# Kernel optimization log

Hardware: AMD Instinct MI355X
Metric: run time of the kernel (lower is better)

Reference implementation:

```python
import jax, jax.numpy as jnp
import numpy as np

HID = 2048
HEADS = 16
HD = HID // HEADS  # 128
EPS = 1e-6


def setup_inputs() -> dict:
    key = jax.random.key(0)
    ks = jax.random.split(key, 9)
    s = 1.0 / np.sqrt(HID)
    return {
        "hidden_states": jax.random.normal(ks[0], (4, 4096, HID), jnp.float32),
        "q_w": jax.random.normal(ks[1], (HID, HID), jnp.float32) * s,
        "q_b": jnp.zeros((HID,), jnp.float32),
        "k_w": jax.random.normal(ks[2], (HID, HID), jnp.float32) * s,
        "k_b": jnp.zeros((HID,), jnp.float32),
        "v_w": jax.random.normal(ks[3], (HID, HID), jnp.float32) * s,
        "v_b": jnp.zeros((HID,), jnp.float32),
        "o_w": jax.random.normal(ks[4], (HID, HID), jnp.float32) * s,
        "o_b": jnp.zeros((HID,), jnp.float32),
    }


def _heads(x, b, s):
    # [B,S,HID] -> [B,H,S,Dh]
    return x.reshape(b, s, HEADS, HD).transpose(0, 2, 1, 3)


def reference(hidden_states, q_w, q_b, k_w, k_b, v_w, v_b, o_w, o_b):
    b, s, _ = hidden_states.shape
    # torch Linear: y = x @ W.T + b
    q = _heads(hidden_states @ q_w.T + q_b, b, s)
    k = _heads(hidden_states @ k_w.T + k_b, b, s)
    v = _heads(hidden_states @ v_w.T + v_b, b, s)
    # kernel feature map: elu(x) + 1
    qp = jax.nn.elu(q) + 1.0
    kp = jax.nn.elu(k) + 1.0
    # KV outer-product reduction over sequence: [B,H,Dh,Dh]
    kv = jnp.einsum('bhsd,bhse->bhde', kp, v)
    # normalizer z = q' @ sum_s k'  -> [B,H,S,1]
    z = jnp.einsum('bhsd,bhd->bhs', qp, kp.sum(axis=2))[..., None]
    attn = jnp.einsum('bhsd,bhde->bhse', qp, kv) / (z + EPS)
    out = attn.transpose(0, 2, 1, 3).reshape(b, s, HID)
    return out @ o_w.T + o_b
```

## Files before the change

### kernel.cpp

```cpp
#include <hip/hip_runtime.h>
#include <hip/hip_bf16.h>

#define HIDC 2048
#define NHEADS 16
#define HDIM 128
#define NB 4
#define NS 4096
#define NROWS (NB*NS)
#define QSTR 6144
#define EPSV 1e-6f

typedef __attribute__((ext_vector_type(8))) short s16x8;
typedef __attribute__((ext_vector_type(4))) float f32x4;
typedef __attribute__((ext_vector_type(8))) unsigned short u16x8;

static __device__ __forceinline__ unsigned short f2b(float f) {
  unsigned int u = __float_as_uint(f);
  u += 0x7fffu + ((u >> 16) & 1u);
  return (unsigned short)(u >> 16);
}
static __device__ __forceinline__ float b2f(unsigned short h) {
  return __uint_as_float(((unsigned int)h) << 16);
}

static __device__ __forceinline__ void gload_lds16(const unsigned short* g, unsigned short* l) {
  __builtin_amdgcn_global_load_lds(
      (const __attribute__((address_space(1))) void*)g,
      (__attribute__((address_space(3))) void*)l, 16, 0, 0);
}

__global__ __launch_bounds__(256) void convert_all(
    const float* __restrict__ hs, const float* __restrict__ qw,
    const float* __restrict__ kw, const float* __restrict__ vw,
    const float* __restrict__ ow,
    unsigned short* __restrict__ hsb, unsigned short* __restrict__ qwb,
    unsigned short* __restrict__ kwb, unsigned short* __restrict__ vwb,
    unsigned short* __restrict__ owb)
{
  int bid = blockIdx.x;
  const float* src; unsigned short* dst; size_t base;
  if (bid < 16384) { src = hs; dst = hsb; base = (size_t)bid << 11; }
  else {
    int t = bid - 16384; int wsel = t >> 11; int wb = t & 2047;
    src = wsel == 0 ? qw : wsel == 1 ? kw : wsel == 2 ? vw : ow;
    dst = wsel == 0 ? qwb : wsel == 1 ? kwb : wsel == 2 ? vwb : owb;
    base = (size_t)wb << 11;
  }
  size_t i = base + ((size_t)threadIdx.x << 3);
  float4 a = *(const float4*)(src + i);
  float4 b = *(const float4*)(src + i + 4);
  u16x8 o;
  o[0] = f2b(a.x); o[1] = f2b(a.y); o[2] = f2b(a.z); o[3] = f2b(a.w);
  o[4] = f2b(b.x); o[5] = f2b(b.y); o[6] = f2b(b.z); o[7] = f2b(b.w);
  *(u16x8*)(dst + i) = o;
}

template<int QKV, int OUT_BF16>
__global__ __launch_bounds__(512, 2) void gemm256(
    const unsigned short* __restrict__ A,
    const unsigned short* __restrict__ B0,
    const unsigned short* __restrict__ B1,
    const unsigned short* __restrict__ B2,
    const float* __restrict__ bias0,
    const float* __restrict__ bias1,
    const float* __restrict__ bias2,
    void* __restrict__ Cp,
    int ntile, int astr, int ostr)
{
  __shared__ unsigned short lds[65536];
  const int tid = threadIdx.x;
  const int lane = tid & 63, wid = tid >> 6;
  const int wr = wid >> 2, wc = wid & 3;
  const int l15 = lane & 15, l4 = lane >> 4;

  const int cpx = (int)gridDim.x >> 3;
  const int bidx = (int)blockIdx.x;
  const int wg = (bidx & 7) * cpx + (bidx >> 3);
  const int csz = ntile << 2;
  const int chunk = wg / csz;
  const int t = wg % csz;
  const int bm = ((chunk << 2) + (t & 3)) << 8;
  const int bn = (t >> 2) << 8;

  const unsigned short* Bp = B0;
  const float* bias = bias0;
  bool act = false;
  int bnw = bn;
  if (QKV) {
    int seg = bn >> 11;
    Bp = seg == 0 ? B0 : (seg == 1 ? B1 : B2);
    bias = seg == 0 ? bias0 : (seg == 1 ? bias1 : bias2);
    act = seg < 2;
    bnw = bn & 2047;
  }

  const int c0 = wid << 1;
  const int srow = lane >> 2;
  const int scol = (((lane & 3) ^ ((srow >> 1) & 3)) << 3);
  const unsigned short* Asrc0 = A + (size_t)(bm + (c0 << 4) + srow) * astr + scol;
  const unsigned short* Asrc1 = Asrc0 + (size_t)16 * astr;
  const unsigned short* Bsrc0 = Bp + (size_t)(bnw + (c0 << 4) + srow) * HIDC + scol;
  const unsigned short* Bsrc1 = Bsrc0 + (size_t)16 * HIDC;
  const int adst = c0 << 9;

  const int xa = ((l4 ^ ((l15 >> 1) & 3)) << 3);
  const int abase = ((wr << 7) + l15) * 32 + xa;
  const int bbase = 8192 + ((wc << 6) + l15) * 32 + xa;

  f32x4 acc[8][4] = {};
  s16x8 af[2][8];
  s16x8 bfr[4];

#define STAGE_A(s_) { const int sl_ = ((s_) & 3) << 14; const int kt_ = (s_) << 5; \
    gload_lds16(Asrc0 + kt_, &lds[sl_ + adst]); \
    gload_lds16(Asrc1 + kt_, &lds[sl_ + adst + 512]); }
#define STAGE_B(s_) { const int sl_ = ((s_) & 3) << 14; const int kt_ = (s_) << 5; \
    gload_lds16(Bsrc0 + kt_, &lds[sl_ + 8192 + adst]); \
    gload_lds16(Bsrc1 + kt_, &lds[sl_ + 8192 + adst + 512]); }

#define MM8(nf_, P_) { \
    acc[0][nf_] = __builtin_amdgcn_mfma_f32_16x16x32_bf16(af[P_][0], bfr[nf_], acc[0][nf_], 0, 0, 0); \
    acc[1][nf_] = __builtin_amdgcn_mfma_f32_16x16x32_bf16(af[P_][1], bfr[nf_], acc[1][nf_], 0, 0, 0); \
    acc[2][nf_] = __builtin_amdgcn_mfma_f32_16x16x32_bf16(af[P_][2], bfr[nf_], acc[2][nf_], 0, 0, 0); \
    acc[3][nf_] = __builtin_amdgcn_mfma_f32_16x16x32_bf16(af[P_][3], bfr[nf_], acc[3][nf_], 0, 0, 0); \
    acc[4][nf_] = __builtin_amdgcn_mfma_f32_16x16x32_bf16(af[P_][4], bfr[nf_], acc[4][nf_], 0, 0, 0); \
    acc[5][nf_] = __builtin_amdgcn_mfma_f32_16x16x32_bf16(af[P_][5], bfr[nf_], acc[5][nf_], 0, 0, 0); \
    acc[6][nf_] = __builtin_amdgcn_mfma_f32_16x16x32_bf16(af[P_][6], bfr[nf_], acc[6][nf_], 0, 0, 0); \
    acc[7][nf_] = __builtin_amdgcn_mfma_f32_16x16x32_bf16(af[P_][7], bfr[nf_], acc[7][nf_], 0, 0, 0); }

#define DO_STEP(s_, P_, GATE, DO_A, DO_STG) { \
    const int sl = ((s_) & 3) << 14; \
    if ((GATE) == 4)      { asm volatile("s_waitcnt vmcnt(4)" ::: "memory"); } \
    else if ((GATE) == 0) { asm volatile("s_waitcnt vmcnt(0)" ::: "memory"); } \
    __builtin_amdgcn_s_barrier(); \
    bfr[0] = *(const s16x8*)&lds[sl + bbase]; \
    bfr[1] = *(const s16x8*)&lds[sl + bbase + 512]; \
    bfr[2] = *(const s16x8*)&lds[sl + bbase + 1024]; \
    bfr[3] = *(const s16x8*)&lds[sl + bbase + 1536]; \
    if (DO_A) { \
      const int sln = (((s_) + 1) & 3) << 14; \
      af[1-(P_)][0] = *(const s16x8*)&lds[sln + abase]; \
      af[1-(P_)][1] = *(const s16x8*)&lds[sln + abase + 512]; \
      af[1-(P_)][2] = *(const s16x8*)&lds[sln + abase + 1024]; \
      af[1-(P_)][3] = *(const s16x8*)&lds[sln + abase + 1536]; \
      af[1-(P_)][4] = *(const s16x8*)&lds[sln + abase + 2048]; \
      af[1-(P_)][5] = *(const s16x8*)&lds[sln + abase + 2560]; \
      af[1-(P_)][6] = *(const s16x8*)&lds[sln + abase + 3072]; \
      af[1-(P_)][7] = *(const s16x8*)&lds[sln + abase + 3584]; \
    } \
    if (DO_STG) { STAGE_A((s_) + 3); STAGE_B((s_) + 3); } \
    __builtin_amdgcn_sched_barrier(0); \
    __builtin_amdgcn_s_setprio(1); \
    MM8(0, P_) MM8(1, P_) MM8(2, P_) MM8(3, P_) \
    __builtin_amdgcn_s_setprio(0); \
  }

  STAGE_A(0); STAGE_B(0);
  STAGE_A(1); STAGE_B(1);
  STAGE_A(2); STAGE_B(2);
  asm volatile("s_waitcnt vmcnt(8)" ::: "memory");
  __builtin_amdgcn_s_barrier();
  af[0][0] = *(const s16x8*)&lds[abase];
  af[0][1] = *(const s16x8*)&lds[abase + 512];
  af[0][2] = *(const s16x8*)&lds[abase + 1024];
  af[0][3] = *(const s16x8*)&lds[abase + 1536];
  af[0][4] = *(const s16x8*)&lds[abase + 2048];
  af[0][5] = *(const s16x8*)&lds[abase + 2560];
  af[0][6] = *(const s16x8*)&lds[abase + 3072];
  af[0][7] = *(const s16x8*)&lds[abase + 3584];

  for (int s = 0; s < 60; s += 2) {
    DO_STEP(s,     0, 4, 1, 1)
    DO_STEP(s + 1, 1, 4, 1, 1)
  }
  DO_STEP(60, 0, 4, 1, 1)
  DO_STEP(61, 1, 4, 1, 0)
  DO_STEP(62, 0, 0, 1, 0)
  DO_STEP(63, 1, -1, 0, 0)

#undef DO_STEP
#undef MM8
#undef STAGE_A
#undef STAGE_B

  #pragma unroll
  for (int nf = 0; nf < 4; ++nf) {
    const int colw = (wc << 6) + (nf << 4) + l15;
    const float bv = bias[bnw + colw];
    #pragma unroll
    for (int mf = 0; mf < 8; ++mf) {
      #pragma unroll
      for (int r = 0; r < 4; ++r) {
        const int row = bm + (wr << 7) + (mf << 4) + (l4 << 2) + r;
        float v = acc[mf][nf][r] + bv;
        if (QKV) { if (act) v = (v > 0.f) ? (v + 1.f) : __expf(v); }
        const size_t off = (size_t)row * ostr + bn + colw;
        if (OUT_BF16) ((unsigned short*)Cp)[off] = f2b(v);
        else          ((float*)Cp)[off] = v;
      }
    }
  }
}

__global__ __launch_bounds__(256) void kv_partial(
    const unsigned short* __restrict__ kp, const unsigned short* __restrict__ vv,
    float* __restrict__ kvp, float* __restrict__ ksp)
{
  const int bh = blockIdx.x >> 4;
  const int chunk = blockIdx.x & 15;
  const int b = bh >> 4, h = bh & 15;
  const int tid = threadIdx.x;
  const int td = tid >> 4, te = tid & 15;

  __shared__ float kpl[32][128];
  __shared__ float vl[32][132];

  float acc[8][8] = {};
  float ks[8] = {};

  const size_t rowbase = (size_t)b * NS * QSTR + (size_t)h * HDIM;
  const int s0 = chunk * 256;

  for (int st = 0; st < 256; st += 32) {
    __syncthreads();
    #pragma unroll
    for (int i = 0; i < 2; ++i) {
      int idx = tid + (i << 8);
      int row = idx >> 4, q = idx & 15;
      size_t g = rowbase + (size_t)(s0 + st + row) * QSTR + (q << 3);
      u16x8 k8 = *(const u16x8*)(kp + g);
      u16x8 v8 = *(const u16x8*)(vv + g);
      float tk[8], tv[8];
      #pragma unroll
      for (int j = 0; j < 8; ++j) { tk[j] = b2f(k8[j]); tv[j] = b2f(v8[j]); }
      *(float4*)&kpl[row][(q << 3)]     = make_float4(tk[0], tk[1], tk[2], tk[3]);
      *(float4*)&kpl[row][(q << 3) + 4] = make_float4(tk[4], tk[5], tk[6], tk[7]);
      *(float4*)&vl[row][(q << 3)]      = make_float4(tv[0], tv[1], tv[2], tv[3]);
      *(float4*)&vl[row][(q << 3) + 4]  = make_float4(tv[4], tv[5], tv[6], tv[7]);
    }
    __syncthreads();
    #pragma unroll 4
    for (int s = 0; s < 32; ++s) {
      float kd[8], ve[8];
      *(float4*)&kd[0] = *(const float4*)&kpl[s][td << 3];
      *(float4*)&kd[4] = *(const float4*)&kpl[s][(td << 3) + 4];
      *(float4*)&ve[0] = *(const float4*)&vl[s][te << 3];
      *(float4*)&ve[4] = *(const float4*)&vl[s][(te << 3) + 4];
      if (te == 0) {
        #pragma unroll
        for (int i = 0; i < 8; ++i) ks[i] += kd[i];
      }
      #pragma unroll
      for (int i = 0; i < 8; ++i)
        #pragma unroll
        for (int j = 0; j < 8; ++j)
          acc[i][j] += kd[i] * ve[j];
    }
  }

  float* outp = kvp + ((size_t)(chunk * 64 + bh) << 14);
  #pragma unroll
  for (int j = 0; j < 8; ++j) {
    int e = (te << 3) + j;
    float r0[8];
    #pragma unroll
    for (int i = 0; i < 8; ++i) r0[i] = acc[i][j];
    *(float4*)&outp[(size_t)e * HDIM + (td << 3)]     = *(float4*)&r0[0];
    *(float4*)&outp[(size_t)e * HDIM + (td << 3) + 4] = *(float4*)&r0[4];
  }
  if (te == 0) {
    float* kso = ksp + ((size_t)(chunk * 64 + bh) << 7) + (td << 3);
    #pragma unroll
    for (int i = 0; i < 8; ++i) kso[i] = ks[i];
  }
}

__global__ __launch_bounds__(256) void kv_reduce(
    const float* __restrict__ kvp, float* __restrict__ kvT)
{
  int i = blockIdx.x * 256 + threadIdx.x;
  float s = 0.f;
  #pragma unroll
  for (int c = 0; c < 16; ++c) s += kvp[(size_t)c * (64 * 16384) + i];
  kvT[i] = s;
}

__global__ __launch_bounds__(256) void attn_ker(
    const unsigned short* __restrict__ qp, const float* __restrict__ kvT,
    const float* __restrict__ ksp, unsigned short* __restrict__ attn)
{
  const int bh = blockIdx.x >> 5, stile = blockIdx.x & 31;
  const int b = bh >> 4, h = bh & 15;
  const int tid = threadIdx.x;
  const int lane = tid & 63, w = tid >> 6;
  const int l15 = lane & 15, l4 = lane >> 4;

  __shared__ unsigned short Qs[128][136];
  __shared__ unsigned short Ks[128][136];
  __shared__ float ksl[128];
  __shared__ float zs[128];

  const size_t qbase = ((size_t)b * NS + (size_t)stile * 128) * QSTR + (size_t)h * HDIM;

  #pragma unroll
  for (int i = 0; i < 8; ++i) {
    int idx = tid + (i << 8);
    int row = idx >> 4, q = idx & 15;
    u16x8 v8 = *(const u16x8*)(qp + qbase + (size_t)row * QSTR + (q << 3));
    *(u16x8*)&Qs[row][q << 3] = v8;
  }
  const float* kvb = kvT + ((size_t)bh << 14);
  #pragma unroll
  for (int i = 0; i < 16; ++i) {
    int idx = tid + (i << 8);
    int row = idx >> 5, q = idx & 31;
    float4 v4 = *(const float4*)(kvb + (size_t)row * HDIM + (q << 2));
    ushort4 w4; w4.x = f2b(v4.x); w4.y = f2b(v4.y); w4.z = f2b(v4.z); w4.w = f2b(v4.w);
    *(ushort4*)&Ks[row][q << 2] = w4;
  }
  if (tid < 128) {
    float s = 0.f;
    #pragma unroll
    for (int c = 0; c < 16; ++c) s += ksp[((size_t)(c * 64 + bh) << 7) + tid];
    ksl[tid] = s;
  }
  __syncthreads();
  if (tid < 128) {
    float z = 0.f;
    #pragma unroll
    for (int dq = 0; dq < 16; ++dq) {
      u16x8 qv = *(const u16x8*)&Qs[tid][dq << 3];
      #pragma unroll
      for (int j = 0; j < 8; ++j) z += b2f(qv[j]) * ksl[(dq << 3) + j];
    }
    zs[tid] = 1.f / (z + EPSV);
  }
  __syncthreads();

  f32x4 acc[2][8] = {};
  #pragma unroll
  for (int kk = 0; kk < 4; ++kk) {
    s16x8 a[2], bb[8];
    #pragma unroll
    for (int mf = 0; mf < 2; ++mf)
      a[mf] = *(const s16x8*)&Qs[(w << 5) + (mf << 4) + l15][(kk << 5) + (l4 << 3)];
    #pragma unroll
    for (int nf = 0; nf < 8; ++nf)
      bb[nf] = *(const s16x8*)&Ks[(nf << 4) + l15][(kk << 5) + (l4 << 3)];
    #pragma unroll
    for (int mf = 0; mf < 2; ++mf)
      #pragma unroll
      for (int nf = 0; nf < 8; ++nf)
        acc[mf][nf] = __builtin_amdgcn_mfma_f32_16x16x32_bf16(a[mf], bb[nf], acc[mf][nf], 0, 0, 0);
  }

  #pragma unroll
  for (int mf = 0; mf < 2; ++mf) {
    #pragma unroll
    for (int r = 0; r < 4; ++r) {
      const int rl = (w << 5) + (mf << 4) + (l4 << 2) + r;
      const float zi = zs[rl];
      #pragma unroll
      for (int nf = 0; nf < 8; ++nf) {
        const int e = (nf << 4) + l15;
        attn[qbase + (size_t)rl * QSTR + e] = f2b(acc[mf][nf][r] * zi);
      }
    }
  }
}

extern "C" void kernel_launch(void* const* d_in, const int* in_sizes, int n_in,
                              void* d_out, int out_size, void* d_ws, size_t ws_size,
                              hipStream_t stream) {
  const float* hs = (const float*)d_in[0];
  const float* qw = (const float*)d_in[1];
  const float* qb = (const float*)d_in[2];
  const float* kw = (const float*)d_in[3];
  const float* kb = (const float*)d_in[4];
  const float* vw = (const float*)d_in[5];
  const float* vb = (const float*)d_in[6];
  const float* ow = (const float*)d_in[7];
  const float* ob = (const float*)d_in[8];

  char* w = (char*)d_ws;
  unsigned short* hsb = (unsigned short*)(w);
  unsigned short* qwb = (unsigned short*)(w + 67108864);
  unsigned short* kwb = (unsigned short*)(w + 75497472);
  unsigned short* vwb = (unsigned short*)(w + 83886080);
  unsigned short* owb = (unsigned short*)(w + 92274688);
  unsigned short* qkv = (unsigned short*)(w + 100663296);
  float* kvp = (float*)(w);
  float* ksp = (float*)(w + 67108864);
  float* kvT = (float*)(w + 67108864 + 524288);

  convert_all<<<dim3(24576), dim3(256), 0, stream>>>(hs, qw, kw, vw, ow, hsb, qwb, kwb, vwb, owb);
  gemm256<1, 1><<<dim3(24 * 64), dim3(512), 0, stream>>>(
      hsb, qwb, kwb, vwb, qb, kb, vb, qkv, 24, HIDC, QSTR);
  kv_partial<<<dim3(1024), dim3(256), 0, stream>>>(qkv + 2048, qkv + 4096, kvp, ksp);
  kv_reduce<<<dim3(4096), dim3(256), 0, stream>>>(kvp, kvT);
  attn_ker<<<dim3(2048), dim3(256), 0, stream>>>(qkv, kvT, ksp, qkv + 4096);
  gemm256<0, 0><<<dim3(8 * 64), dim3(512), 0, stream>>>(
      qkv + 4096, owb, owb, owb, ob, ob, ob, d_out, 8, QSTR, HIDC);
}
```

Baseline: 777.5 us.

## Shrink GEMM tile to 256x128 with 4 waves and triple-buffered LDS

```diff
diff --git a/kernel.cpp b/kernel.cpp
--- a/kernel.cpp
+++ b/kernel.cpp
@@ -56,7 +56,7 @@
 }
 
 template<int QKV, int OUT_BF16>
-__global__ __launch_bounds__(512, 2) void gemm256(
+__global__ __launch_bounds__(256, 2) void gemm256(
     const unsigned short* __restrict__ A,
     const unsigned short* __restrict__ B0,
     const unsigned short* __restrict__ B1,
@@ -67,10 +67,10 @@
     void* __restrict__ Cp,
     int ntile, int astr, int ostr)
 {
-  __shared__ unsigned short lds[65536];
+  __shared__ unsigned short lds[36864];
   const int tid = threadIdx.x;
   const int lane = tid & 63, wid = tid >> 6;
-  const int wr = wid >> 2, wc = wid & 3;
+  const int wr = wid >> 1, wc = wid & 1;
   const int l15 = lane & 15, l4 = lane >> 4;
 
   const int cpx = (int)gridDim.x >> 3;
@@ -80,7 +80,7 @@
   const int chunk = wg / csz;
   const int t = wg % csz;
   const int bm = ((chunk << 2) + (t & 3)) << 8;
-  const int bn = (t >> 2) << 8;
+  const int bn = (t >> 2) << 7;
 
   const unsigned short* Bp = B0;
   const float* bias = bias0;
@@ -94,94 +94,76 @@
     bnw = bn & 2047;
   }
 
-  const int c0 = wid << 1;
   const int srow = lane >> 2;
   const int scol = (((lane & 3) ^ ((srow >> 1) & 3)) << 3);
-  const unsigned short* Asrc0 = A + (size_t)(bm + (c0 << 4) + srow) * astr + scol;
+  const unsigned short* Asrc0 = A + (size_t)(bm + ((wid << 2) << 4) + srow) * astr + scol;
   const unsigned short* Asrc1 = Asrc0 + (size_t)16 * astr;
-  const unsigned short* Bsrc0 = Bp + (size_t)(bnw + (c0 << 4) + srow) * HIDC + scol;
+  const unsigned short* Asrc2 = Asrc0 + (size_t)32 * astr;
+  const unsigned short* Asrc3 = Asrc0 + (size_t)48 * astr;
+  const unsigned short* Bsrc0 = Bp + (size_t)(bnw + ((wid << 1) << 4) + srow) * HIDC + scol;
   const unsigned short* Bsrc1 = Bsrc0 + (size_t)16 * HIDC;
-  const int adst = c0 << 9;
+  const int adst = wid << 11;
+  const int bdst = 8192 + (wid << 10);
 
   const int xa = ((l4 ^ ((l15 >> 1) & 3)) << 3);
   const int abase = ((wr << 7) + l15) * 32 + xa;
   const int bbase = 8192 + ((wc << 6) + l15) * 32 + xa;
 
   f32x4 acc[8][4] = {};
-  s16x8 af[2][8];
-  s16x8 bfr[4];
-
-#define STAGE_A(s_) { const int sl_ = ((s_) & 3) << 14; const int kt_ = (s_) << 5; \
-    gload_lds16(Asrc0 + kt_, &lds[sl_ + adst]); \
-    gload_lds16(Asrc1 + kt_, &lds[sl_ + adst + 512]); }
-#define STAGE_B(s_) { const int sl_ = ((s_) & 3) << 14; const int kt_ = (s_) << 5; \
-    gload_lds16(Bsrc0 + kt_, &lds[sl_ + 8192 + adst]); \
-    gload_lds16(Bsrc1 + kt_, &lds[sl_ + 8192 + adst + 512]); }
-
-#define MM8(nf_, P_) { \
-    acc[0][nf_] = __builtin_amdgcn_mfma_f32_16x16x32_bf16(af[P_][0], bfr[nf_], acc[0][nf_], 0, 0, 0); \
-    acc[1][nf_] = __builtin_amdgcn_mfma_f32_16x16x32_bf16(af[P_][1], bfr[nf_], acc[1][nf_], 0, 0, 0); \
-    acc[2][nf_] = __builtin_amdgcn_mfma_f32_16x16x32_bf16(af[P_][2], bfr[nf_], acc[2][nf_], 0, 0, 0); \
-    acc[3][nf_] = __builtin_amdgcn_mfma_f32_16x16x32_bf16(af[P_][3], bfr[nf_], acc[3][nf_], 0, 0, 0); \
-    acc[4][nf_] = __builtin_amdgcn_mfma_f32_16x16x32_bf16(af[P_][4], bfr[nf_], acc[4][nf_], 0, 0, 0); \
-    acc[5][nf_] = __builtin_amdgcn_mfma_f32_16x16x32_bf16(af[P_][5], bfr[nf_], acc[5][nf_], 0, 0, 0); \
-    acc[6][nf_] = __builtin_amdgcn_mfma_f32_16x16x32_bf16(af[P_][6], bfr[nf_], acc[6][nf_], 0, 0, 0); \
-    acc[7][nf_] = __builtin_amdgcn_mfma_f32_16x16x32_bf16(af[P_][7], bfr[nf_], acc[7][nf_], 0, 0, 0); }
-
-#define DO_STEP(s_, P_, GATE, DO_A, DO_STG) { \
-    const int sl = ((s_) & 3) << 14; \
-    if ((GATE) == 4)      { asm volatile("s_waitcnt vmcnt(4)" ::: "memory"); } \
+  s16x8 af[8], bfr[4];
+
+#define STAGE6(sb_, kt_) { \
+    gload_lds16(Asrc0 + (kt_), &lds[(sb_) + adst]); \
+    gload_lds16(Asrc1 + (kt_), &lds[(sb_) + adst + 512]); \
+    gload_lds16(Asrc2 + (kt_), &lds[(sb_) + adst + 1024]); \
+    gload_lds16(Asrc3 + (kt_), &lds[(sb_) + adst + 1536]); \
+    gload_lds16(Bsrc0 + (kt_), &lds[(sb_) + bdst]); \
+    gload_lds16(Bsrc1 + (kt_), &lds[(sb_) + bdst + 512]); }
+
+#define MMROW(mf_) { \
+    acc[mf_][0] = __builtin_amdgcn_mfma_f32_16x16x32_bf16(af[mf_], bfr[0], acc[mf_][0], 0, 0, 0); \
+    acc[mf_][1] = __builtin_amdgcn_mfma_f32_16x16x32_bf16(af[mf_], bfr[1], acc[mf_][1], 0, 0, 0); \
+    acc[mf_][2] = __builtin_amdgcn_mfma_f32_16x16x32_bf16(af[mf_], bfr[2], acc[mf_][2], 0, 0, 0); \
+    acc[mf_][3] = __builtin_amdgcn_mfma_f32_16x16x32_bf16(af[mf_], bfr[3], acc[mf_][3], 0, 0, 0); }
+
+#define DO_STEP(GATE, STG, KT) { \
+    if ((GATE) == 6)      { asm volatile("s_waitcnt vmcnt(6)" ::: "memory"); } \
     else if ((GATE) == 0) { asm volatile("s_waitcnt vmcnt(0)" ::: "memory"); } \
     __builtin_amdgcn_s_barrier(); \
-    bfr[0] = *(const s16x8*)&lds[sl + bbase]; \
-    bfr[1] = *(const s16x8*)&lds[sl + bbase + 512]; \
-    bfr[2] = *(const s16x8*)&lds[sl + bbase + 1024]; \
-    bfr[3] = *(const s16x8*)&lds[sl + bbase + 1536]; \
-    if (DO_A) { \
-      const int sln = (((s_) + 1) & 3) << 14; \
-      af[1-(P_)][0] = *(const s16x8*)&lds[sln + abase]; \
-      af[1-(P_)][1] = *(const s16x8*)&lds[sln + abase + 512]; \
-      af[1-(P_)][2] = *(const s16x8*)&lds[sln + abase + 1024]; \
-      af[1-(P_)][3] = *(const s16x8*)&lds[sln + abase + 1536]; \
-      af[1-(P_)][4] = *(const s16x8*)&lds[sln + abase + 2048]; \
-      af[1-(P_)][5] = *(const s16x8*)&lds[sln + abase + 2560]; \
-      af[1-(P_)][6] = *(const s16x8*)&lds[sln + abase + 3072]; \
-      af[1-(P_)][7] = *(const s16x8*)&lds[sln + abase + 3584]; \
-    } \
-    if (DO_STG) { STAGE_A((s_) + 3); STAGE_B((s_) + 3); } \
+    bfr[0] = *(const s16x8*)&lds[rb + bbase]; \
+    bfr[1] = *(const s16x8*)&lds[rb + bbase + 512]; \
+    bfr[2] = *(const s16x8*)&lds[rb + bbase + 1024]; \
+    bfr[3] = *(const s16x8*)&lds[rb + bbase + 1536]; \
+    af[0] = *(const s16x8*)&lds[rb + abase]; \
+    af[1] = *(const s16x8*)&lds[rb + abase + 512]; \
+    af[2] = *(const s16x8*)&lds[rb + abase + 1024]; \
+    af[3] = *(const s16x8*)&lds[rb + abase + 1536]; \
+    af[4] = *(const s16x8*)&lds[rb + abase + 2048]; \
+    af[5] = *(const s16x8*)&lds[rb + abase + 2560]; \
+    af[6] = *(const s16x8*)&lds[rb + abase + 3072]; \
+    af[7] = *(const s16x8*)&lds[rb + abase + 3584]; \
+    if (STG) STAGE6(sb, KT); \
     __builtin_amdgcn_sched_barrier(0); \
     __builtin_amdgcn_s_setprio(1); \
-    MM8(0, P_) MM8(1, P_) MM8(2, P_) MM8(3, P_) \
+    MMROW(0) MMROW(1) MMROW(2) MMROW(3) \
+    MMROW(4) MMROW(5) MMROW(6) MMROW(7) \
     __builtin_amdgcn_s_setprio(0); \
-  }
-
-  STAGE_A(0); STAGE_B(0);
-  STAGE_A(1); STAGE_B(1);
-  STAGE_A(2); STAGE_B(2);
-  asm volatile("s_waitcnt vmcnt(8)" ::: "memory");
-  __builtin_amdgcn_s_barrier();
-  af[0][0] = *(const s16x8*)&lds[abase];
-  af[0][1] = *(const s16x8*)&lds[abase + 512];
-  af[0][2] = *(const s16x8*)&lds[abase + 1024];
-  af[0][3] = *(const s16x8*)&lds[abase + 1536];
-  af[0][4] = *(const s16x8*)&lds[abase + 2048];
-  af[0][5] = *(const s16x8*)&lds[abase + 2560];
-  af[0][6] = *(const s16x8*)&lds[abase + 3072];
-  af[0][7] = *(const s16x8*)&lds[abase + 3584];
-
-  for (int s = 0; s < 60; s += 2) {
-    DO_STEP(s,     0, 4, 1, 1)
-    DO_STEP(s + 1, 1, 4, 1, 1)
-  }
-  DO_STEP(60, 0, 4, 1, 1)
-  DO_STEP(61, 1, 4, 1, 0)
-  DO_STEP(62, 0, 0, 1, 0)
-  DO_STEP(63, 1, -1, 0, 0)
+    { int t_ = rb; rb = (rb == 24576) ? 0 : rb + 12288; sb = t_; } \
+  }
+
+  STAGE6(0, 0);
+  STAGE6(12288, 32);
+  int rb = 0, sb = 24576;
+
+  for (int s = 0; s < 62; ++s) {
+    DO_STEP(6, 1, (s + 2) << 5)
+  }
+  DO_STEP(0, 0, 0)
+  DO_STEP(-1, 0, 0)
 
 #undef DO_STEP
-#undef MM8
-#undef STAGE_A
-#undef STAGE_B
+#undef MMROW
+#undef STAGE6
 
   #pragma unroll
   for (int nf = 0; nf < 4; ++nf) {
@@ -394,11 +376,11 @@
   float* kvT = (float*)(w + 67108864 + 524288);
 
   convert_all<<<dim3(24576), dim3(256), 0, stream>>>(hs, qw, kw, vw, ow, hsb, qwb, kwb, vwb, owb);
-  gemm256<1, 1><<<dim3(24 * 64), dim3(512), 0, stream>>>(
-      hsb, qwb, kwb, vwb, qb, kb, vb, qkv, 24, HIDC, QSTR);
+  gemm256<1, 1><<<dim3(3072), dim3(256), 0, stream>>>(
+      hsb, qwb, kwb, vwb, qb, kb, vb, qkv, 48, HIDC, QSTR);
   kv_partial<<<dim3(1024), dim3(256), 0, stream>>>(qkv + 2048, qkv + 4096, kvp, ksp);
   kv_reduce<<<dim3(4096), dim3(256), 0, stream>>>(kvp, kvT);
   attn_ker<<<dim3(2048), dim3(256), 0, stream>>>(qkv, kvT, ksp, qkv + 4096);
-  gemm256<0, 0><<<dim3(8 * 64), dim3(512), 0, stream>>>(
-      qkv + 4096, owb, owb, owb, ob, ob, ob, d_out, 8, QSTR, HIDC);
-}
+  gemm256<0, 0><<<dim3(1024), dim3(256), 0, stream>>>(
+      qkv + 4096, owb, owb, owb, ob, ob, ob, d_out, 16, QSTR, HIDC);
+}
```

Result: slower. 805.5 us (+3.6%).
